# Kernel tuning notes

Measured on AMD Instinct MI355X. Metric: run time of the kernel, lower is better.

Reference implementation:

```python
import jax, jax.numpy as jnp
import numpy as np

EMBED = 512
HID = 16
BATCH = 4
SEQ = 1024


def setup_inputs() -> dict:
    key = jax.random.key(0)
    ks = jax.random.split(key, 8)
    e, h = EMBED, HID
    inputs = jax.random.normal(ks[0], (BATCH, SEQ, e), dtype=jnp.float32)
    # nn.Linear default init ~ U(-1/sqrt(fan_in), 1/sqrt(fan_in)); approximate scale
    Wq = jax.random.normal(ks[1], (e, e), dtype=jnp.float32) / np.sqrt(e)
    Wk = jax.random.normal(ks[2], (e, e), dtype=jnp.float32) / np.sqrt(e)
    Wv = jax.random.normal(ks[3], (e, e), dtype=jnp.float32) / np.sqrt(e)
    W1 = jax.random.normal(ks[4], (h, 2 * e), dtype=jnp.float32) / np.sqrt(2 * e)
    b1 = jnp.zeros((h,), dtype=jnp.float32)
    w2 = jax.random.normal(ks[5], (h,), dtype=jnp.float32) / np.sqrt(h)
    b2 = jnp.zeros((1,), dtype=jnp.float32)
    return {"inputs": inputs, "Wq": Wq, "Wk": Wk, "Wv": Wv,
            "W1": W1, "b1": b1, "w2": w2, "b2": b2}


def reference(inputs, Wq, Wk, Wv, W1, b1, w2, b2):
    e = inputs.shape[-1]
    # projections (torch Linear: x @ W.T)
    q = jnp.einsum('bse,fe->bsf', inputs, Wq)
    k = jnp.einsum('bse,fe->bsf', inputs, Wk)
    v = jnp.einsum('bse,fe->bsf', inputs, Wv)
    # attn_net Linear over concat [q_i; k_j] factorizes:
    # W1 @ [q;k] = W1[:, :e] @ q_i + W1[:, e:] @ k_j
    A = jnp.einsum('bse,he->bsh', q, W1[:, :e]) + b1  # (b, s, h)
    B = jnp.einsum('bse,he->bsh', k, W1[:, e:])       # (b, s, h)
    hidden = jnp.tanh(A[:, :, None, :] + B[:, None, :, :])  # (b, s, s, h)
    logits = jnp.einsum('bijh,h->bij', hidden, w2) + b2[0]   # (b, s, s)
    attn = jax.nn.softmax(logits, axis=-1)
    return jnp.einsum('bij,bjd->bid', attn, v)
```

## Files before the change

### kernel.cpp

```cpp
#include <hip/hip_runtime.h>
#include <math.h>
#include <stdint.h>

#define EMBED 512
#define HID 16
#define SEQ 1024

typedef unsigned short u16;
typedef __attribute__((ext_vector_type(8))) __bf16 bf16x8;
typedef __attribute__((ext_vector_type(4))) float f32x4;

__device__ __forceinline__ u16 f2bf(float f) {
    unsigned u = __float_as_uint(f);
    unsigned r = (u + 0x7FFFu + ((u >> 16) & 1u)) >> 16;
    return (u16)r;
}
__device__ __forceinline__ float bf2f(u16 h) {
    return __uint_as_float(((unsigned)h) << 16);
}
__device__ __forceinline__ void gload16(const void* g, void* d) {
    __builtin_amdgcn_global_load_lds(
        reinterpret_cast<const __attribute__((address_space(1))) unsigned int*>(
            reinterpret_cast<uintptr_t>(g)),
        reinterpret_cast<__attribute__((address_space(3))) unsigned int*>(
            reinterpret_cast<uintptr_t>(d)),
        16, 0, 0);
}

__global__ __launch_bounds__(256) void wc_kernel(
    const float* __restrict__ Wq, const float* __restrict__ Wk,
    const float* __restrict__ W1, const float* __restrict__ Wvm,
    float* __restrict__ WcT, u16* __restrict__ wv_hi, u16* __restrict__ wv_lo)
{
    __shared__ float w1s[EMBED];
    int t = threadIdx.x;
    if (blockIdx.x >= 64) {
        int i = (blockIdx.x - 64) * 256 + t;
        float4 v = ((const float4*)Wvm)[i];
        u16 h0 = f2bf(v.x), h1 = f2bf(v.y), h2 = f2bf(v.z), h3 = f2bf(v.w);
        ((ushort4*)wv_hi)[i] = make_ushort4(h0, h1, h2, h3);
        ((ushort4*)wv_lo)[i] = make_ushort4(f2bf(v.x - bf2f(h0)), f2bf(v.y - bf2f(h1)),
                                            f2bf(v.z - bf2f(h2)), f2bf(v.w - bf2f(h3)));
        return;
    }
    int h2 = blockIdx.x >> 1;
    int ab = h2 >> 4, h = h2 & 15;
    const float* Wmat = ab ? Wk : Wq;
    const float* w1row = W1 + (size_t)h * (2 * EMBED) + ab * EMBED;
    for (int f = t; f < EMBED; f += 256) w1s[f] = w1row[f];
    __syncthreads();
    int e0 = ((blockIdx.x & 1) << 8) + t;
    float acc = 0.f;
    #pragma unroll 16
    for (int f = 0; f < EMBED; ++f)
        acc += w1s[f] * Wmat[(size_t)f * EMBED + e0];
    WcT[(size_t)e0 * 32 + h2] = acc;
}

__global__ __launch_bounds__(256) void ab_kernel(
    const float* __restrict__ x, const float* __restrict__ WcT,
    const float* __restrict__ b1,
    float* __restrict__ EA, float* __restrict__ EB, u16* __restrict__ x_hi)
{
    const float K2 = 2.8853900817779268f;
    __shared__ float xs[8][EMBED];
    __shared__ float wcs[EMBED * 32];
    int t = threadIdx.x;
    int s0 = blockIdx.x * 8;
    #pragma unroll
    for (int i = 0; i < 4; ++i) {
        int idx = t + i * 256;
        int row = idx >> 7, c4 = idx & 127;
        float4 vv = *(const float4*)(x + (size_t)(s0 + row) * EMBED + c4 * 4);
        *(float4*)&xs[row][c4 * 4] = vv;
        u16 h0 = f2bf(vv.x), h1 = f2bf(vv.y), h2 = f2bf(vv.z), h3 = f2bf(vv.w);
        ((ushort4*)x_hi)[(s0 + row) * 128 + c4] = make_ushort4(h0, h1, h2, h3);
    }
    #pragma unroll
    for (int i = 0; i < 16; ++i) {
        int idx = t + i * 256;
        ((float4*)wcs)[idx] = ((const float4*)WcT)[idx];
    }
    __syncthreads();
    int r = t >> 5, h2 = t & 31;
    const float* xr = xs[r];
    float acc = 0.f;
    #pragma unroll 8
    for (int k = 0; k < EMBED; ++k)
        acc += xr[k] * wcs[k * 32 + h2];
    int s = s0 + r;
    if (h2 < HID)
        EA[(size_t)s * HID + h2] = __builtin_amdgcn_exp2f(K2 * (acc + b1[h2]));
    else
        EB[(size_t)s * HID + (h2 - 16)] = __builtin_amdgcn_exp2f(K2 * acc);
}

template<int NR>
__device__ __forceinline__ void stageR(const u16* src, int ld, int kt,
                                       u16* ldsb, int t)
{
    int kb0 = kt << 7;
    #pragma unroll
    for (int i = 0; i < NR / 32; ++i) {
        int row  = i * 32 + (t >> 3);
        int colb = (((t & 7) ^ ((t >> 3) & 7)) << 4);
        const char* g = (const char*)src + (size_t)row * ((size_t)ld * 2) + kb0 + colb;
        gload16(g, (char*)ldsb + i * 4096 + ((t >> 6) << 10) + ((t & 63) << 4));
    }
}
__device__ __forceinline__ bf16x8 ldfrag(const u16* ldsb, int r, int s) {
    return *(const bf16x8*)((const char*)ldsb + r * 128 + (((s ^ (r & 7))) << 4));
}

__global__ __launch_bounds__(256, 4) void vgemm_kernel(
    const u16* __restrict__ Ah, const u16* __restrict__ Al,
    const u16* __restrict__ Bh, u16* __restrict__ outH)
{
    constexpr int TOFF = 64 * 64;
    __shared__ __attribute__((aligned(16))) u16 lds[3 * TOFF];
    int t = threadIdx.x;
    int l = t & 63, wid = t >> 6;
    int wm = (wid >> 1) * 32, wn = (wid & 1) * 32;
    int m0 = blockIdx.y * 64, n0 = blockIdx.x * 64;
    const u16* pAh = Ah + (size_t)m0 * EMBED;
    const u16* pAl = Al + (size_t)m0 * EMBED;
    const u16* pBh = Bh + (size_t)n0 * EMBED;
    f32x4 acc[2][2] = {};

    for (int kt = 0; kt < 8; ++kt) {
        stageR<64>(pAh, EMBED, kt, lds, t);
        stageR<64>(pAl, EMBED, kt, lds + TOFF, t);
        stageR<64>(pBh, EMBED, kt, lds + 2 * TOFF, t);
        __syncthreads();
        #pragma unroll
        for (int kk = 0; kk < 2; ++kk) {
            int sb = (kk << 2) + (l >> 4);
            bf16x8 ah[2], al2[2], bh[2];
            #pragma unroll
            for (int mf = 0; mf < 2; ++mf) {
                int r = wm + mf * 16 + (l & 15);
                ah[mf]  = ldfrag(lds, r, sb);
                al2[mf] = ldfrag(lds + TOFF, r, sb);
            }
            #pragma unroll
            for (int nf = 0; nf < 2; ++nf)
                bh[nf] = ldfrag(lds + 2 * TOFF, wn + nf * 16 + (l & 15), sb);
            #pragma unroll
            for (int mf = 0; mf < 2; ++mf)
                #pragma unroll
                for (int nf = 0; nf < 2; ++nf) {
                    acc[mf][nf] = __builtin_amdgcn_mfma_f32_16x16x32_bf16(ah[mf],  bh[nf], acc[mf][nf], 0, 0, 0);
                    acc[mf][nf] = __builtin_amdgcn_mfma_f32_16x16x32_bf16(al2[mf], bh[nf], acc[mf][nf], 0, 0, 0);
                }
        }
        __syncthreads();
    }

    int cr = (l >> 4) << 2, cc = l & 15;
    #pragma unroll
    for (int mf = 0; mf < 2; ++mf)
        #pragma unroll
        for (int nf = 0; nf < 2; ++nf)
            #pragma unroll
            for (int r = 0; r < 4; ++r)
                outH[(size_t)(m0 + wm + mf * 16 + cr + r) * 4096
                     + n0 + wn + nf * 16 + cc] = f2bf(acc[mf][nf][r]);
}

__global__ __launch_bounds__(256) void attn_kernel(
    const float* __restrict__ EA, const float* __restrict__ EB,
    const float* __restrict__ w2, u16* __restrict__ P)
{
    const float L2E = 1.4426950408889634f;
    __shared__ float redA[4], redB[4];
    int blk = blockIdx.x;
    int b = blk >> 9;
    int i0 = (blk & 511) << 1;
    int t = threadIdx.x;

    const float4* ArA = (const float4*)(EA + (size_t)(b * SEQ + i0) * HID);
    const float4* ArB = (const float4*)(EA + (size_t)(b * SEQ + i0 + 1) * HID);
    float4 X0 = ArA[0], X1 = ArA[1], X2 = ArA[2], X3 = ArA[3];
    float4 Y0 = ArB[0], Y1 = ArB[1], Y2 = ArB[2], Y3 = ArB[3];

    const float4* Wq4 = (const float4*)w2;
    float4 u0 = Wq4[0], u1 = Wq4[1], u2 = Wq4[2], u3 = Wq4[3];
    float Pa1 = -2.f*u0.x, Pa2 = -2.f*u0.y, Pas = Pa1 + Pa2;
    float Pb1 = -2.f*u0.z, Pb2 = -2.f*u0.w, Pbs = Pb1 + Pb2;
    float Pc1 = -2.f*u1.x, Pc2 = -2.f*u1.y, Pcs = Pc1 + Pc2;
    float Pd1 = -2.f*u1.z, Pd2 = -2.f*u1.w, Pds = Pd1 + Pd2;
    float Pe1 = -2.f*u2.x, Pe2 = -2.f*u2.y, Pes = Pe1 + Pe2;
    float Pf1 = -2.f*u2.z, Pf2 = -2.f*u2.w, Pfs = Pf1 + Pf2;
    float Pg1 = -2.f*u3.x, Pg2 = -2.f*u3.y, Pgs = Pg1 + Pg2;
    float Ph1 = -2.f*u3.z, Ph2 = -2.f*u3.w, Phs = Ph1 + Ph2;
    float S0 = fmaxf(Pa1,0.f)+fmaxf(Pa2,0.f)+fmaxf(Pb1,0.f)+fmaxf(Pb2,0.f)
             + fmaxf(Pc1,0.f)+fmaxf(Pc2,0.f)+fmaxf(Pd1,0.f)+fmaxf(Pd2,0.f)
             + fmaxf(Pe1,0.f)+fmaxf(Pe2,0.f)+fmaxf(Pf1,0.f)+fmaxf(Pf2,0.f)
             + fmaxf(Pg1,0.f)+fmaxf(Pg2,0.f)+fmaxf(Ph1,0.f)+fmaxf(Ph2,0.f);

#define QUAD(AV, BV, P1, P2, PS12, P3, P4, PS34) { \
    float e1 = AV.x * BV.x, e2 = AV.y * BV.y, e3 = AV.z * BV.z, e4 = AV.w * BV.w; \
    float D12 = fmaf(e1, e2, e1) + (e2 + 1.0f); \
    float N12 = fmaf((P2), e1, fmaf((P1), e2, (PS12))); \
    float D34 = fmaf(e3, e4, e3) + (e4 + 1.0f); \
    float N34 = fmaf((P4), e3, fmaf((P3), e4, (PS34))); \
    float Dq = D12 * D34; \
    float Nq = fmaf(N12, D34, N34 * D12); \
    s = fmaf(Nq, __builtin_amdgcn_rcpf(Dq), s); }

#define CALCLG(LG, W0, W1_, W2_, W3_, v0, v1, v2, v3) { float s = 0.f; \
    QUAD(W0,  v0, Pa1, Pa2, Pas, Pb1, Pb2, Pbs) \
    QUAD(W1_, v1, Pc1, Pc2, Pcs, Pd1, Pd2, Pds) \
    QUAD(W2_, v2, Pe1, Pe2, Pes, Pf1, Pf2, Pfs) \
    QUAD(W3_, v3, Pg1, Pg2, Pgs, Ph1, Ph2, Phs) \
    LG = s; }

    const float* EBB = EB + (size_t)(b << 10) * HID;
    float pa0, pa1, pa2, pa3, pb0, pb1, pb2, pb3;

#define DOC(c, PA, PB) { \
    const float4* q = (const float4*)(EBB + (size_t)(t + (c) * 256) * HID); \
    float4 v0 = q[0], v1 = q[1], v2 = q[2], v3 = q[3]; \
    float lgA, lgB; \
    CALCLG(lgA, X0, X1, X2, X3, v0, v1, v2, v3) \
    CALCLG(lgB, Y0, Y1, Y2, Y3, v0, v1, v2, v3) \
    PA = __builtin_amdgcn_exp2f((lgA - S0) * L2E); \
    PB = __builtin_amdgcn_exp2f((lgB - S0) * L2E); }

    DOC(0, pa0, pb0)
    DOC(1, pa1, pb1)
    DOC(2, pa2, pb2)
    DOC(3, pa3, pb3)
#undef DOC
#undef CALCLG
#undef QUAD

    float sA = (pa0 + pa1) + (pa2 + pa3);
    float sB = (pb0 + pb1) + (pb2 + pb3);
    #pragma unroll
    for (int o = 32; o > 0; o >>= 1) {
        sA += __shfl_xor(sA, o);
        sB += __shfl_xor(sB, o);
    }
    if ((t & 63) == 0) { redA[t >> 6] = sA; redB[t >> 6] = sB; }
    __syncthreads();
    float invA = __fdividef(1.f, (redA[0] + redA[1]) + (redA[2] + redA[3]));
    float invB = __fdividef(1.f, (redB[0] + redB[1]) + (redB[2] + redB[3]));

    size_t baseA = ((size_t)(b * SEQ) + i0) * SEQ;
    size_t baseB = baseA + SEQ;
    P[baseA + t      ] = f2bf(pa0 * invA);
    P[baseA + t + 256] = f2bf(pa1 * invA);
    P[baseA + t + 512] = f2bf(pa2 * invA);
    P[baseA + t + 768] = f2bf(pa3 * invA);
    P[baseB + t      ] = f2bf(pb0 * invB);
    P[baseB + t + 256] = f2bf(pb1 * invB);
    P[baseB + t + 512] = f2bf(pb2 * invB);
    P[baseB + t + 768] = f2bf(pb3 * invB);
}

__global__ __launch_bounds__(256, 2) void pv_kernel(
    const u16* __restrict__ P, const u16* __restrict__ VT,
    float* __restrict__ out)
{
    constexpr int AOFF = 128 * 64;
    constexpr int BOFF = 64 * 64;
    constexpr int BUFW = AOFF + BOFF;
    __shared__ __attribute__((aligned(16))) u16 lds[2 * BUFW];
    int t = threadIdx.x;
    int l = t & 63, wid = t >> 6;
    int wm = (wid >> 1) * 64, wn = (wid & 1) * 32;
    int m0 = blockIdx.y * 128, n0 = blockIdx.x * 64;
    int zb = blockIdx.z;
    const u16* pA = P + (size_t)zb * SEQ * SEQ + (size_t)m0 * SEQ;
    const u16* pB = VT + (size_t)n0 * 4096 + ((size_t)zb << 10);

    f32x4 acc[4][2] = {};

    auto STAGE = [&](int buf, int kt) {
        u16* base = lds + buf * BUFW;
        stageR<128>(pA, SEQ, kt, base, t);
        stageR<64>(pB, 4096, kt, base + AOFF, t);
    };
    auto COMPUTE = [&](int buf) {
        u16* lA = lds + buf * BUFW;
        u16* lB = lA + AOFF;
        #pragma unroll
        for (int kk = 0; kk < 2; ++kk) {
            int sb = (kk << 2) + (l >> 4);
            bf16x8 af[4], bf_[2];
            #pragma unroll
            for (int mf = 0; mf < 4; ++mf)
                af[mf] = ldfrag(lA, wm + mf * 16 + (l & 15), sb);
            #pragma unroll
            for (int nf = 0; nf < 2; ++nf)
                bf_[nf] = ldfrag(lB, wn + nf * 16 + (l & 15), sb);
            #pragma unroll
            for (int mf = 0; mf < 4; ++mf)
                #pragma unroll
                for (int nf = 0; nf < 2; ++nf)
                    acc[mf][nf] = __builtin_amdgcn_mfma_f32_16x16x32_bf16(af[mf], bf_[nf], acc[mf][nf], 0, 0, 0);
        }
    };

    STAGE(0, 0);
    __syncthreads();
    int cur = 0;
    for (int kt = 0; kt + 1 < 16; ++kt) {
        STAGE(cur ^ 1, kt + 1);
        COMPUTE(cur);
        __syncthreads();
        cur ^= 1;
    }
    COMPUTE(cur);

    int cr = (l >> 4) << 2, cc = l & 15;
    #pragma unroll
    for (int mf = 0; mf < 4; ++mf)
        #pragma unroll
        for (int nf = 0; nf < 2; ++nf)
            #pragma unroll
            for (int r = 0; r < 4; ++r)
                out[((size_t)(zb * SEQ) + m0 + wm + mf * 16 + cr + r) * EMBED
                    + n0 + wn + nf * 16 + cc] = acc[mf][nf][r];
}

extern "C" void kernel_launch(void* const* d_in, const int* in_sizes, int n_in,
                              void* d_out, int out_size, void* d_ws, size_t ws_size,
                              hipStream_t stream) {
    const float* x   = (const float*)d_in[0];
    const float* Wq  = (const float*)d_in[1];
    const float* Wk  = (const float*)d_in[2];
    const float* Wvm = (const float*)d_in[3];
    const float* W1  = (const float*)d_in[4];
    const float* b1  = (const float*)d_in[5];
    const float* w2  = (const float*)d_in[6];

    char* ws = (char*)d_ws;
    float* WcT   = (float*)(ws + 0);
    float* EA    = (float*)(ws + 65536);
    float* EB    = (float*)(ws + 327680);
    u16*   VT_hi = (u16*)(ws + 589824);
    u16*   x_hi  = (u16*)(ws + 4784128);
    u16*   wv_hi = (u16*)(ws + 8978432);
    u16*   wv_lo = (u16*)(ws + 9502720);
    u16*   P     = (u16*)(ws + 10027008);
    float* out   = (float*)d_out;

    hipLaunchKernelGGL(wc_kernel, dim3(320), dim3(256), 0, stream,
                       Wq, Wk, W1, Wvm, WcT, wv_hi, wv_lo);
    hipLaunchKernelGGL(ab_kernel, dim3(512), dim3(256), 0, stream,
                       x, WcT, b1, EA, EB, x_hi);
    hipLaunchKernelGGL(vgemm_kernel, dim3(64, 8), dim3(256), 0, stream,
                       wv_hi, wv_lo, x_hi, VT_hi);
    hipLaunchKernelGGL(attn_kernel, dim3(2048), dim3(256), 0, stream,
                       EA, EB, w2, P);
    hipLaunchKernelGGL(pv_kernel, dim3(8, 8, 4), dim3(256), 0, stream,
                       P, VT_hi, out);
}
```

Measured before the change: 65.23 us.

## Fold attention-score projections into the V-projection MFMA GEMM and drop ab_kernel

Stores the combined W1·Wq and W1·Wk rows as extra split-bf16 rows under the Wv matrix, so one MFMA GEMM (grid 64x9) produces V^T along with the transposed exp(2·A) and exp(2·B) tables. This removes the separate scalar fp32 ab_kernel launch and its large LDS staging. The attention kernel now reads the transposed EA/EB layout, with coalesced per-h loads across j. The trade-off is that the A/B projections now use bf16 hi/lo precision instead of fp32, plus extra padded GEMM rows and a larger prep grid.

Measured after the change: 60.66 us. -7.0%, faster.

```diff
diff --git a/kernel.cpp b/kernel.cpp
--- a/kernel.cpp
+++ b/kernel.cpp
@@ -27,72 +27,44 @@
         16, 0, 0);
 }
 
-__global__ __launch_bounds__(256) void wc_kernel(
+__global__ __launch_bounds__(256) void prep_kernel(
     const float* __restrict__ Wq, const float* __restrict__ Wk,
     const float* __restrict__ W1, const float* __restrict__ Wvm,
-    float* __restrict__ WcT, u16* __restrict__ wv_hi, u16* __restrict__ wv_lo)
+    const float* __restrict__ x,
+    u16* __restrict__ AH, u16* __restrict__ AL, u16* __restrict__ x_hi)
 {
     __shared__ float w1s[EMBED];
     int t = threadIdx.x;
-    if (blockIdx.x >= 64) {
-        int i = (blockIdx.x - 64) * 256 + t;
+    int blk = blockIdx.x;
+    if (blk < 64) {
+        int h2 = blk >> 1, half = blk & 1;
+        int ab = h2 >> 4, h = h2 & 15;
+        const float* Wmat = ab ? Wk : Wq;
+        const float* w1row = W1 + (size_t)h * (2 * EMBED) + ab * EMBED;
+        for (int f = t; f < EMBED; f += 256) w1s[f] = w1row[f];
+        __syncthreads();
+        int e0 = (half << 8) + t;
+        float acc = 0.f;
+        #pragma unroll 16
+        for (int f = 0; f < EMBED; ++f)
+            acc += w1s[f] * Wmat[(size_t)f * EMBED + e0];
+        u16 hi = f2bf(acc);
+        AH[(size_t)(512 + h2) * EMBED + e0] = hi;
+        AL[(size_t)(512 + h2) * EMBED + e0] = f2bf(acc - bf2f(hi));
+        AH[(size_t)(544 + h2) * EMBED + e0] = 0;
+        AL[(size_t)(544 + h2) * EMBED + e0] = 0;
+    } else if (blk < 320) {
+        int i = (blk - 64) * 256 + t;
         float4 v = ((const float4*)Wvm)[i];
         u16 h0 = f2bf(v.x), h1 = f2bf(v.y), h2 = f2bf(v.z), h3 = f2bf(v.w);
-        ((ushort4*)wv_hi)[i] = make_ushort4(h0, h1, h2, h3);
-        ((ushort4*)wv_lo)[i] = make_ushort4(f2bf(v.x - bf2f(h0)), f2bf(v.y - bf2f(h1)),
-                                            f2bf(v.z - bf2f(h2)), f2bf(v.w - bf2f(h3)));
-        return;
-    }
-    int h2 = blockIdx.x >> 1;
-    int ab = h2 >> 4, h = h2 & 15;
-    const float* Wmat = ab ? Wk : Wq;
-    const float* w1row = W1 + (size_t)h * (2 * EMBED) + ab * EMBED;
-    for (int f = t; f < EMBED; f += 256) w1s[f] = w1row[f];
-    __syncthreads();
-    int e0 = ((blockIdx.x & 1) << 8) + t;
-    float acc = 0.f;
-    #pragma unroll 16
-    for (int f = 0; f < EMBED; ++f)
-        acc += w1s[f] * Wmat[(size_t)f * EMBED + e0];
-    WcT[(size_t)e0 * 32 + h2] = acc;
-}
-
-__global__ __launch_bounds__(256) void ab_kernel(
-    const float* __restrict__ x, const float* __restrict__ WcT,
-    const float* __restrict__ b1,
-    float* __restrict__ EA, float* __restrict__ EB, u16* __restrict__ x_hi)
-{
-    const float K2 = 2.8853900817779268f;
-    __shared__ float xs[8][EMBED];
-    __shared__ float wcs[EMBED * 32];
-    int t = threadIdx.x;
-    int s0 = blockIdx.x * 8;
-    #pragma unroll
-    for (int i = 0; i < 4; ++i) {
-        int idx = t + i * 256;
-        int row = idx >> 7, c4 = idx & 127;
-        float4 vv = *(const float4*)(x + (size_t)(s0 + row) * EMBED + c4 * 4);
-        *(float4*)&xs[row][c4 * 4] = vv;
-        u16 h0 = f2bf(vv.x), h1 = f2bf(vv.y), h2 = f2bf(vv.z), h3 = f2bf(vv.w);
-        ((ushort4*)x_hi)[(s0 + row) * 128 + c4] = make_ushort4(h0, h1, h2, h3);
-    }
-    #pragma unroll
-    for (int i = 0; i < 16; ++i) {
-        int idx = t + i * 256;
-        ((float4*)wcs)[idx] = ((const float4*)WcT)[idx];
-    }
-    __syncthreads();
-    int r = t >> 5, h2 = t & 31;
-    const float* xr = xs[r];
-    float acc = 0.f;
-    #pragma unroll 8
-    for (int k = 0; k < EMBED; ++k)
-        acc += xr[k] * wcs[k * 32 + h2];
-    int s = s0 + r;
-    if (h2 < HID)
-        EA[(size_t)s * HID + h2] = __builtin_amdgcn_exp2f(K2 * (acc + b1[h2]));
-    else
-        EB[(size_t)s * HID + (h2 - 16)] = __builtin_amdgcn_exp2f(K2 * acc);
+        ((ushort4*)AH)[i] = make_ushort4(h0, h1, h2, h3);
+        ((ushort4*)AL)[i] = make_ushort4(f2bf(v.x - bf2f(h0)), f2bf(v.y - bf2f(h1)),
+                                         f2bf(v.z - bf2f(h2)), f2bf(v.w - bf2f(h3)));
+    } else {
+        int i = (blk - 320) * 256 + t;
+        float4 v = ((const float4*)x)[i];
+        ((ushort4*)x_hi)[i] = make_ushort4(f2bf(v.x), f2bf(v.y), f2bf(v.z), f2bf(v.w));
+    }
 }
 
 template<int NR>
@@ -112,18 +84,20 @@
     return *(const bf16x8*)((const char*)ldsb + r * 128 + (((s ^ (r & 7))) << 4));
 }
 
-__global__ __launch_bounds__(256, 4) void vgemm_kernel(
-    const u16* __restrict__ Ah, const u16* __restrict__ Al,
-    const u16* __restrict__ Bh, u16* __restrict__ outH)
-{
+__global__ __launch_bounds__(256, 4) void gemm_kernel(
+    const u16* __restrict__ AH, const u16* __restrict__ AL,
+    const u16* __restrict__ Bh, const float* __restrict__ b1,
+    u16* __restrict__ VT, float* __restrict__ EAt, float* __restrict__ EBt)
+{
+    const float K2 = 2.8853900817779268f;
     constexpr int TOFF = 64 * 64;
     __shared__ __attribute__((aligned(16))) u16 lds[3 * TOFF];
     int t = threadIdx.x;
     int l = t & 63, wid = t >> 6;
     int wm = (wid >> 1) * 32, wn = (wid & 1) * 32;
     int m0 = blockIdx.y * 64, n0 = blockIdx.x * 64;
-    const u16* pAh = Ah + (size_t)m0 * EMBED;
-    const u16* pAl = Al + (size_t)m0 * EMBED;
+    const u16* pAh = AH + (size_t)m0 * EMBED;
+    const u16* pAl = AL + (size_t)m0 * EMBED;
     const u16* pBh = Bh + (size_t)n0 * EMBED;
     f32x4 acc[2][2] = {};
 
@@ -162,13 +136,24 @@
         #pragma unroll
         for (int nf = 0; nf < 2; ++nf)
             #pragma unroll
-            for (int r = 0; r < 4; ++r)
-                outH[(size_t)(m0 + wm + mf * 16 + cr + r) * 4096
-                     + n0 + wn + nf * 16 + cc] = f2bf(acc[mf][nf][r]);
+            for (int r = 0; r < 4; ++r) {
+                int gr = m0 + wm + mf * 16 + cr + r;
+                int col = n0 + wn + nf * 16 + cc;
+                float v = acc[mf][nf][r];
+                if (gr < 512) {
+                    VT[(size_t)gr * 4096 + col] = f2bf(v);
+                } else if (gr < 528) {
+                    EAt[(size_t)(gr - 512) * 4096 + col] =
+                        __builtin_amdgcn_exp2f(K2 * (v + b1[gr - 512]));
+                } else if (gr < 544) {
+                    EBt[(size_t)(gr - 528) * 4096 + col] =
+                        __builtin_amdgcn_exp2f(K2 * v);
+                }
+            }
 }
 
 __global__ __launch_bounds__(256) void attn_kernel(
-    const float* __restrict__ EA, const float* __restrict__ EB,
+    const float* __restrict__ EAt, const float* __restrict__ EBt,
     const float* __restrict__ w2, u16* __restrict__ P)
 {
     const float L2E = 1.4426950408889634f;
@@ -177,63 +162,60 @@
     int b = blk >> 9;
     int i0 = (blk & 511) << 1;
     int t = threadIdx.x;
-
-    const float4* ArA = (const float4*)(EA + (size_t)(b * SEQ + i0) * HID);
-    const float4* ArB = (const float4*)(EA + (size_t)(b * SEQ + i0 + 1) * HID);
-    float4 X0 = ArA[0], X1 = ArA[1], X2 = ArA[2], X3 = ArA[3];
-    float4 Y0 = ArB[0], Y1 = ArB[1], Y2 = ArB[2], Y3 = ArB[3];
-
-    const float4* Wq4 = (const float4*)w2;
-    float4 u0 = Wq4[0], u1 = Wq4[1], u2 = Wq4[2], u3 = Wq4[3];
-    float Pa1 = -2.f*u0.x, Pa2 = -2.f*u0.y, Pas = Pa1 + Pa2;
-    float Pb1 = -2.f*u0.z, Pb2 = -2.f*u0.w, Pbs = Pb1 + Pb2;
-    float Pc1 = -2.f*u1.x, Pc2 = -2.f*u1.y, Pcs = Pc1 + Pc2;
-    float Pd1 = -2.f*u1.z, Pd2 = -2.f*u1.w, Pds = Pd1 + Pd2;
-    float Pe1 = -2.f*u2.x, Pe2 = -2.f*u2.y, Pes = Pe1 + Pe2;
-    float Pf1 = -2.f*u2.z, Pf2 = -2.f*u2.w, Pfs = Pf1 + Pf2;
-    float Pg1 = -2.f*u3.x, Pg2 = -2.f*u3.y, Pgs = Pg1 + Pg2;
-    float Ph1 = -2.f*u3.z, Ph2 = -2.f*u3.w, Phs = Ph1 + Ph2;
-    float S0 = fmaxf(Pa1,0.f)+fmaxf(Pa2,0.f)+fmaxf(Pb1,0.f)+fmaxf(Pb2,0.f)
-             + fmaxf(Pc1,0.f)+fmaxf(Pc2,0.f)+fmaxf(Pd1,0.f)+fmaxf(Pd2,0.f)
-             + fmaxf(Pe1,0.f)+fmaxf(Pe2,0.f)+fmaxf(Pf1,0.f)+fmaxf(Pf2,0.f)
-             + fmaxf(Pg1,0.f)+fmaxf(Pg2,0.f)+fmaxf(Ph1,0.f)+fmaxf(Ph2,0.f);
-
-#define QUAD(AV, BV, P1, P2, PS12, P3, P4, PS34) { \
-    float e1 = AV.x * BV.x, e2 = AV.y * BV.y, e3 = AV.z * BV.z, e4 = AV.w * BV.w; \
-    float D12 = fmaf(e1, e2, e1) + (e2 + 1.0f); \
-    float N12 = fmaf((P2), e1, fmaf((P1), e2, (PS12))); \
-    float D34 = fmaf(e3, e4, e3) + (e4 + 1.0f); \
-    float N34 = fmaf((P4), e3, fmaf((P3), e4, (PS34))); \
-    float Dq = D12 * D34; \
-    float Nq = fmaf(N12, D34, N34 * D12); \
-    s = fmaf(Nq, __builtin_amdgcn_rcpf(Dq), s); }
-
-#define CALCLG(LG, W0, W1_, W2_, W3_, v0, v1, v2, v3) { float s = 0.f; \
-    QUAD(W0,  v0, Pa1, Pa2, Pas, Pb1, Pb2, Pbs) \
-    QUAD(W1_, v1, Pc1, Pc2, Pcs, Pd1, Pd2, Pds) \
-    QUAD(W2_, v2, Pe1, Pe2, Pes, Pf1, Pf2, Pfs) \
-    QUAD(W3_, v3, Pg1, Pg2, Pgs, Ph1, Ph2, Phs) \
-    LG = s; }
-
-    const float* EBB = EB + (size_t)(b << 10) * HID;
+    int gA = (b << 10) + i0;
+
+    float ax[HID], ay[HID];
+    #pragma unroll
+    for (int h = 0; h < HID; ++h) {
+        ax[h] = EAt[(size_t)h * 4096 + gA];
+        ay[h] = EAt[(size_t)h * 4096 + gA + 1];
+    }
+
+    float P1a[8], P2a[8], PSa[8];
+    #pragma unroll
+    for (int p = 0; p < 8; ++p) {
+        float w1 = -2.f * w2[2 * p], w2_ = -2.f * w2[2 * p + 1];
+        P1a[p] = w1; P2a[p] = w2_; PSa[p] = w1 + w2_;
+    }
+    float S0 = 0.f;
+    #pragma unroll
+    for (int p = 0; p < 8; ++p) S0 += fmaxf(P1a[p], 0.f) + fmaxf(P2a[p], 0.f);
+
+    const float* EBb = EBt + (b << 10);
     float pa0, pa1, pa2, pa3, pb0, pb1, pb2, pb3;
 
 #define DOC(c, PA, PB) { \
-    const float4* q = (const float4*)(EBB + (size_t)(t + (c) * 256) * HID); \
-    float4 v0 = q[0], v1 = q[1], v2 = q[2], v3 = q[3]; \
-    float lgA, lgB; \
-    CALCLG(lgA, X0, X1, X2, X3, v0, v1, v2, v3) \
-    CALCLG(lgB, Y0, Y1, Y2, Y3, v0, v1, v2, v3) \
-    PA = __builtin_amdgcn_exp2f((lgA - S0) * L2E); \
-    PB = __builtin_amdgcn_exp2f((lgB - S0) * L2E); }
+    int j = t + (c) * 256; \
+    float bb[HID]; \
+    _Pragma("unroll") \
+    for (int h = 0; h < HID; ++h) bb[h] = EBb[(size_t)h * 4096 + j]; \
+    float sA = 0.f, sB = 0.f; \
+    _Pragma("unroll") \
+    for (int q = 0; q < 4; ++q) { \
+        int h0 = q << 2, p0 = q << 1, p1 = p0 + 1; \
+        { float e1 = ax[h0]*bb[h0], e2 = ax[h0+1]*bb[h0+1]; \
+          float e3 = ax[h0+2]*bb[h0+2], e4 = ax[h0+3]*bb[h0+3]; \
+          float D12 = fmaf(e1, e2, e1) + (e2 + 1.0f); \
+          float N12 = fmaf(P2a[p0], e1, fmaf(P1a[p0], e2, PSa[p0])); \
+          float D34 = fmaf(e3, e4, e3) + (e4 + 1.0f); \
+          float N34 = fmaf(P2a[p1], e3, fmaf(P1a[p1], e4, PSa[p1])); \
+          sA = fmaf(fmaf(N12, D34, N34 * D12), __builtin_amdgcn_rcpf(D12 * D34), sA); } \
+        { float e1 = ay[h0]*bb[h0], e2 = ay[h0+1]*bb[h0+1]; \
+          float e3 = ay[h0+2]*bb[h0+2], e4 = ay[h0+3]*bb[h0+3]; \
+          float D12 = fmaf(e1, e2, e1) + (e2 + 1.0f); \
+          float N12 = fmaf(P2a[p0], e1, fmaf(P1a[p0], e2, PSa[p0])); \
+          float D34 = fmaf(e3, e4, e3) + (e4 + 1.0f); \
+          float N34 = fmaf(P2a[p1], e3, fmaf(P1a[p1], e4, PSa[p1])); \
+          sB = fmaf(fmaf(N12, D34, N34 * D12), __builtin_amdgcn_rcpf(D12 * D34), sB); } \
+    } \
+    PA = __builtin_amdgcn_exp2f((sA - S0) * L2E); \
+    PB = __builtin_amdgcn_exp2f((sB - S0) * L2E); }
 
     DOC(0, pa0, pb0)
     DOC(1, pa1, pb1)
     DOC(2, pa2, pb2)
     DOC(3, pa3, pb3)
 #undef DOC
-#undef CALCLG
-#undef QUAD
 
     float sA = (pa0 + pa1) + (pa2 + pa3);
     float sB = (pb0 + pb1) + (pb2 + pb3);
@@ -337,24 +319,21 @@
     const float* w2  = (const float*)d_in[6];
 
     char* ws = (char*)d_ws;
-    float* WcT   = (float*)(ws + 0);
-    float* EA    = (float*)(ws + 65536);
-    float* EB    = (float*)(ws + 327680);
-    u16*   VT_hi = (u16*)(ws + 589824);
-    u16*   x_hi  = (u16*)(ws + 4784128);
-    u16*   wv_hi = (u16*)(ws + 8978432);
-    u16*   wv_lo = (u16*)(ws + 9502720);
-    u16*   P     = (u16*)(ws + 10027008);
-    float* out   = (float*)d_out;
-
-    hipLaunchKernelGGL(wc_kernel, dim3(320), dim3(256), 0, stream,
-                       Wq, Wk, W1, Wvm, WcT, wv_hi, wv_lo);
-    hipLaunchKernelGGL(ab_kernel, dim3(512), dim3(256), 0, stream,
-                       x, WcT, b1, EA, EB, x_hi);
-    hipLaunchKernelGGL(vgemm_kernel, dim3(64, 8), dim3(256), 0, stream,
-                       wv_hi, wv_lo, x_hi, VT_hi);
+    u16*   AH   = (u16*)(ws + 0);
+    u16*   AL   = (u16*)(ws + 589824);
+    u16*   x_hi = (u16*)(ws + 1179648);
+    u16*   VT   = (u16*)(ws + 5373952);
+    float* EAt  = (float*)(ws + 9568256);
+    float* EBt  = (float*)(ws + 9830400);
+    u16*   P    = (u16*)(ws + 10092544);
+    float* out  = (float*)d_out;
+
+    hipLaunchKernelGGL(prep_kernel, dim3(2368), dim3(256), 0, stream,
+                       Wq, Wk, W1, Wvm, x, AH, AL, x_hi);
+    hipLaunchKernelGGL(gemm_kernel, dim3(64, 9), dim3(256), 0, stream,
+                       AH, AL, x_hi, b1, VT, EAt, EBt);
     hipLaunchKernelGGL(attn_kernel, dim3(2048), dim3(256), 0, stream,
-                       EA, EB, w2, P);
+                       EAt, EBt, w2, P);
     hipLaunchKernelGGL(pv_kernel, dim3(8, 8, 4), dim3(256), 0, stream,
-                       P, VT_hi, out);
-}
+                       P, VT, out);
+}
```
